# Optimization experiments

Hardware: AMD Instinct MI355X
Metric: run time of the kernel (lower is better)

## Reference

```python
import jax, jax.numpy as jnp
import numpy as np

L = 5        # n_layers
H = 8        # heads
DH = 32      # dim_head = n_hidden // heads
D = 256      # n_hidden
KR = 4       # key_ratio
QKD = KR * DH  # 128, q/k feature dim
IN = 3       # fun_dim + space_dim
OUT = 1      # out_dim
N = 32768    # number of mesh points
EPS = 1e-5

def _ln(x, g, b):
    m = jnp.mean(x, axis=-1, keepdims=True)
    v = jnp.var(x, axis=-1, keepdims=True)
    return (x - m) * jax.lax.rsqrt(v + EPS) * g + b

def _gelu(x):
    return jax.nn.gelu(x, approximate=False)  # torch nn.GELU default (erf)

def setup_inputs() -> dict:
    key = jax.random.key(0)
    ks = iter(jax.random.split(key, 64))
    def w(*s):
        return jax.random.normal(next(ks), s, jnp.float32) * 0.02
    return {
        "x": jax.random.normal(next(ks), (N, IN), jnp.float32),
        # preprocess MLP: Linear(IN,2D)+GELU, Linear(2D,D)
        "pre_w1": w(IN, 2 * D), "pre_b1": jnp.zeros((2 * D,), jnp.float32),
        "pre_w2": w(2 * D, D), "pre_b2": jnp.zeros((D,), jnp.float32),
        "placeholder": jax.random.uniform(next(ks), (D,), jnp.float32) / D,
        # per-block params stacked over L
        "ln1_g": jnp.ones((L, D), jnp.float32), "ln1_b": jnp.zeros((L, D), jnp.float32),
        "inp_w": w(L, D, D), "inp_b": jnp.zeros((L, D), jnp.float32),
        "temp_q": jnp.full((L, H), 0.5, jnp.float32), "temp_k": jnp.full((L, H), 0.5, jnp.float32),
        "wq": w(L, DH, QKD), "wk": w(L, DH, QKD), "wv": w(L, DH, DH),
        "out_w1": w(L, D, D), "out_b1": jnp.zeros((L, D), jnp.float32),
        "out_w2": w(L, D, D), "out_b2": jnp.zeros((L, D), jnp.float32),
        "ln2_g": jnp.ones((L, D), jnp.float32), "ln2_b": jnp.zeros((L, D), jnp.float32),
        "mlp_w1": w(L, D, D), "mlp_b1": jnp.zeros((L, D), jnp.float32),  # mlp_ratio=1 -> hidden=D
        "mlp_w2": w(L, D, D), "mlp_b2": jnp.zeros((L, D), jnp.float32),
        # last-layer head
        "ln3_g": jnp.ones((D,), jnp.float32), "ln3_b": jnp.zeros((D,), jnp.float32),
        "head_w": w(D, OUT), "head_b": jnp.zeros((OUT,), jnp.float32),
    }

def reference(x, pre_w1, pre_b1, pre_w2, pre_b2, placeholder,
              ln1_g, ln1_b, inp_w, inp_b, temp_q, temp_k, wq, wk, wv,
              out_w1, out_b1, out_w2, out_b2, ln2_g, ln2_b,
              mlp_w1, mlp_b1, mlp_w2, mlp_b2, ln3_g, ln3_b, head_w, head_b):
    # preprocess + placeholder bias
    fx = _gelu(x[None] @ pre_w1 + pre_b1) @ pre_w2 + pre_b2  # [1, N, D]
    fx = fx + placeholder
    for i in range(L):
        # --- LinearNO attention block ---
        h = _ln(fx, ln1_g[i], ln1_b[i])
        xm = h @ inp_w[i] + inp_b[i]                       # [1, N, D]
        xm = xm.reshape(1, N, H, DH).transpose(0, 2, 1, 3)  # [1, H, N, DH]
        q = jnp.einsum('bhnd,de->bhne', xm, wq[i])          # [1, H, N, QKD]
        k = jnp.einsum('bhnd,de->bhne', xm, wk[i])          # [1, H, N, QKD]
        v = jnp.einsum('bhnd,dc->bhnc', xm, wv[i])          # [1, H, N, DH]
        tq = jnp.clip(temp_q[i], 0.1, 2.0)[None, :, None, None]
        tk = jnp.clip(temp_k[i], 0.1, 2.0)[None, :, None, None]
        q = jax.nn.softmax(q / tq, axis=-1)  # over feature dim
        k = jax.nn.softmax(k / tk, axis=-2)  # over point dim
        kv = jnp.einsum('bhnd,bhnc->bhdc', k, v)    # [1, H, QKD, DH]
        qkv = jnp.einsum('bhnd,bhdc->bhnc', q, kv)  # [1, H, N, DH]
        qkv = qkv.transpose(0, 2, 1, 3).reshape(1, N, D)
        attn = _gelu(qkv @ out_w1[i] + out_b1[i]) @ out_w2[i] + out_b2[i]
        fx = attn + fx
        # --- MLP block (n_layers=0, res=False: pre + post only) ---
        h2 = _ln(fx, ln2_g[i], ln2_b[i])
        fx = _gelu(h2 @ mlp_w1[i] + mlp_b1[i]) @ mlp_w2[i] + mlp_b2[i] + fx
    # last block head: mlp2(ln_3(fx))
    out = _ln(fx, ln3_g, ln3_b) @ head_w + head_b  # [1, N, OUT]
    return out[0]  # module returns fx[0]
```

## Files before the change

### kernel.cpp

```cpp
#include <hip/hip_runtime.h>
#include <hip/hip_bf16.h>
#include <math.h>

constexpr int NP  = 32768;
constexpr int HH  = 8;

typedef short bf16x8 __attribute__((ext_vector_type(8)));
typedef float f32x4  __attribute__((ext_vector_type(4)));

__device__ __forceinline__ float gelu_f(float x) {
    return 0.5f * x * (1.0f + erff(x * 0.70710678118654752f));
}

__device__ __forceinline__ unsigned short f2bf(float x) {
    union { float f; unsigned u; } v; v.f = x;
    unsigned r = v.u + 0x7fffu + ((v.u >> 16) & 1u);
    return (unsigned short)(r >> 16);
}

__device__ __forceinline__ float bf2f(unsigned short h) {
    union { unsigned u; float f; } v; v.u = ((unsigned)h) << 16;
    return v.f;
}

__global__ __launch_bounds__(256) void transpose_bf16_k(
    const float* __restrict__ src, unsigned short* __restrict__ dst, int K)
{
    __shared__ float tile[32][33];
    int g = blockIdx.z;
    int k0 = blockIdx.x * 32, c0 = blockIdx.y * 32;
    int tx = threadIdx.x & 31, ty = threadIdx.x >> 5;
    const float* s = src + (size_t)g * K * 256;
    unsigned short* d = dst + (size_t)g * 256 * K;
    #pragma unroll
    for (int rr = 0; rr < 4; ++rr) {
        int r = ty + rr * 8;
        tile[r][tx] = s[(size_t)(k0 + r) * 256 + c0 + tx];
    }
    __syncthreads();
    #pragma unroll
    for (int rr = 0; rr < 4; ++rr) {
        int r = ty + rr * 8;
        d[(size_t)(c0 + r) * K + k0 + tx] = f2bf(tile[tx][r]);
    }
}

__global__ __launch_bounds__(256) void transpose_scale_bf16_k(
    const float* __restrict__ src, const float* __restrict__ g,
    unsigned short* __restrict__ dst, int K)
{
    __shared__ float tile[32][33];
    int z = blockIdx.z;
    int k0 = blockIdx.x * 32, c0 = blockIdx.y * 32;
    int tx = threadIdx.x & 31, ty = threadIdx.x >> 5;
    const float* s = src + (size_t)z * K * 256;
    unsigned short* d = dst + (size_t)z * 256 * K;
    #pragma unroll
    for (int rr = 0; rr < 4; ++rr) {
        int r = ty + rr * 8;
        tile[r][tx] = s[(size_t)(k0 + r) * 256 + c0 + tx];
    }
    __syncthreads();
    float gs = g[z * 256 + k0 + tx];
    #pragma unroll
    for (int rr = 0; rr < 4; ++rr) {
        int r = ty + rr * 8;
        d[(size_t)(c0 + r) * K + k0 + tx] = f2bf(gs * tile[tx][r]);
    }
}

__global__ __launch_bounds__(256) void colsum_k(
    const float* __restrict__ W, const float* __restrict__ g,
    const float* __restrict__ b, float* __restrict__ c2, float* __restrict__ c1)
{
    int z = blockIdx.z, c = threadIdx.x;
    const float* Wz = W + (size_t)z * 65536;
    const float* gz = g + z * 256;
    const float* bz = b + z * 256;
    float s2 = 0.f, s1 = 0.f;
    for (int k = 0; k < 256; ++k) {
        float w = Wz[k * 256 + c];
        s2 += gz[k] * w;
        s1 += bz[k] * w;
    }
    c2[z * 256 + c] = s2;
    c1[z * 256 + c] = s1;
}

__global__ __launch_bounds__(256) void prep_wkvT(
    const float* __restrict__ wk, const float* __restrict__ wv,
    const float* __restrict__ wq,
    unsigned short* __restrict__ wkT, unsigned short* __restrict__ wvT,
    unsigned short* __restrict__ wqT)
{
    int l = blockIdx.x, tid = threadIdx.x;
    for (int idx = tid; idx < 4096; idx += 256) {
        int d = idx >> 5, k = idx & 31;
        wkT[l * 4096 + idx] = f2bf(wk[l * 4096 + k * 128 + d]);
        wqT[l * 4096 + idx] = f2bf(wq[l * 4096 + k * 128 + d]);
    }
    for (int idx = tid; idx < 1024; idx += 256) {
        int c = idx >> 5, k = idx & 31;
        wvT[l * 1024 + idx] = f2bf(wv[l * 1024 + k * 32 + c]);
    }
}

template<bool GENA, bool AF32, bool LNFOLD, bool DOGELU, bool RESID, bool STATS, bool PERM>
__global__ __launch_bounds__(256) void gemm_bf(
    const unsigned short* __restrict__ Ah, const float* __restrict__ Af,
    const unsigned short* __restrict__ Wt,
    const float* __restrict__ bias, const float* __restrict__ bias2,
    float* __restrict__ outF, unsigned short* __restrict__ outH,
    const float* __restrict__ stats_in, float* __restrict__ stats_out,
    const float* __restrict__ c1v, const float* __restrict__ c2vec,
    const float* __restrict__ genx, const float* __restrict__ genw1,
    const float* __restrict__ genb1, int K)
{
    __shared__ __align__(16) unsigned short As[128 * 64];
    __shared__ __align__(16) unsigned short Bs[128 * 64];
    __shared__ float rmean[LNFOLD ? 128 : 1];
    __shared__ float rrstd[LNFOLD ? 128 : 1];
    __shared__ float w1s[GENA ? 1536 : 1];
    __shared__ float b1s[GENA ? 512 : 1];
    __shared__ float x3s[GENA ? 512 : 1];

    const int tid = threadIdx.x;
    const int rBase = blockIdx.x * 128, cBase = blockIdx.y * 128;

    if constexpr (GENA) {
        for (int i2 = tid; i2 < 1536; i2 += 256) w1s[i2] = genw1[i2];
        for (int i2 = tid; i2 < 512; i2 += 256) b1s[i2] = genb1[i2];
        if (tid < 128) {
            x3s[tid * 4 + 0] = genx[(size_t)(rBase + tid) * 3 + 0];
            x3s[tid * 4 + 1] = genx[(size_t)(rBase + tid) * 3 + 1];
            x3s[tid * 4 + 2] = genx[(size_t)(rBase + tid) * 3 + 2];
        }
        __syncthreads();
    }
    if constexpr (LNFOLD) {
        if (tid < 128) {
            const float* sp = stats_in + (size_t)(rBase + tid) * 8;
            float4 s0 = *(const float4*)sp;
            float4 s1 = *(const float4*)(sp + 4);
            float mean = (s0.x + s0.z + s1.x + s1.z) * (1.f / 256.f);
            float ex2  = (s0.y + s0.w + s1.y + s1.w) * (1.f / 256.f);
            rmean[tid] = mean;
            rrstd[tid] = rsqrtf(fmaxf(ex2 - mean * mean, 0.f) + 1e-5f);
        }
        __syncthreads();
    }

    f32x4 acc[4][4];
    #pragma unroll
    for (int i = 0; i < 4; ++i)
        #pragma unroll
        for (int j = 0; j < 4; ++j)
            acc[i][j] = (f32x4){0.f, 0.f, 0.f, 0.f};

    const int lane = tid & 63, wid = tid >> 6;
    const int wr = wid >> 1, wc = wid & 1;
    const int lrow = lane & 15, quad = lane >> 4;
    const int srow = tid >> 3;
    const int sch  = tid & 7;

    for (int kc = 0; kc < K; kc += 64) {
        if constexpr (GENA) {
            #pragma unroll
            for (int it = 0; it < 4; ++it) {
                int row = srow + it * 32;
                float x0 = x3s[row * 4 + 0], x1 = x3s[row * 4 + 1], x2 = x3s[row * 4 + 2];
                unsigned short pk[8];
                #pragma unroll
                for (int j = 0; j < 8; ++j) {
                    int k = kc + sch * 8 + j;
                    float t = x0 * w1s[k] + x1 * w1s[512 + k] + x2 * w1s[1024 + k] + b1s[k];
                    pk[j] = f2bf(gelu_f(t));
                }
                *(uint4*)&As[row * 64 + ((sch ^ (row & 7)) << 3)] = *(uint4*)pk;
            }
        } else if constexpr (AF32) {
            #pragma unroll
            for (int it = 0; it < 4; ++it) {
                int row = srow + it * 32;
                const float* ap = Af + (size_t)(rBase + row) * K + kc + sch * 8;
                float4 a0 = *(const float4*)ap;
                float4 a1 = *(const float4*)(ap + 4);
                unsigned short pk[8];
                pk[0] = f2bf(a0.x); pk[1] = f2bf(a0.y); pk[2] = f2bf(a0.z); pk[3] = f2bf(a0.w);
                pk[4] = f2bf(a1.x); pk[5] = f2bf(a1.y); pk[6] = f2bf(a1.z); pk[7] = f2bf(a1.w);
                *(uint4*)&As[row * 64 + ((sch ^ (row & 7)) << 3)] = *(uint4*)pk;
            }
        } else {
            #pragma unroll
            for (int it = 0; it < 4; ++it) {
                int row = srow + it * 32;
                uint4 av = *(const uint4*)(Ah + (size_t)(rBase + row) * K + kc + sch * 8);
                *(uint4*)&As[row * 64 + ((sch ^ (row & 7)) << 3)] = av;
            }
        }
        #pragma unroll
        for (int it = 0; it < 4; ++it) {
            int n = srow + it * 32;
            uint4 wv_ = *(const uint4*)(Wt + (size_t)(cBase + n) * K + kc + sch * 8);
            *(uint4*)&Bs[n * 64 + ((sch ^ (n & 7)) << 3)] = wv_;
        }
        __syncthreads();
        #pragma unroll
        for (int ks = 0; ks < 2; ++ks) {
            bf16x8 af[4], bfr[4];
            #pragma unroll
            for (int t = 0; t < 4; ++t) {
                int row = wr * 64 + t * 16 + lrow;
                af[t] = *(bf16x8*)&As[row * 64 + (((ks * 4 + quad) ^ (row & 7)) << 3)];
                int n = wc * 64 + t * 16 + lrow;
                bfr[t] = *(bf16x8*)&Bs[n * 64 + (((ks * 4 + quad) ^ (n & 7)) << 3)];
            }
            #pragma unroll
            for (int ti = 0; ti < 4; ++ti)
                #pragma unroll
                for (int tj = 0; tj < 4; ++tj)
                    acc[ti][tj] = __builtin_amdgcn_mfma_f32_16x16x32_bf16(
                        af[ti], bfr[tj], acc[ti][tj], 0, 0, 0);
        }
        __syncthreads();
    }

    float c1b[4], c2r[4];
    #pragma unroll
    for (int tj = 0; tj < 4; ++tj) {
        int gcol = cBase + wc * 64 + tj * 16 + lrow;
        float b = bias[gcol];
        if (bias2) b += bias2[gcol];
        if constexpr (LNFOLD) {
            c1b[tj] = c1v[gcol] + b;
            c2r[tj] = c2vec[gcol];
        } else {
            c1b[tj] = b;
            c2r[tj] = 0.f;
        }
    }
    #pragma unroll
    for (int ti = 0; ti < 4; ++ti) {
        #pragma unroll
        for (int r = 0; r < 4; ++r) {
            int rib = wr * 64 + ti * 16 + quad * 4 + r;
            int grow = rBase + rib;
            float mean = 0.f, rstd = 1.f;
            if constexpr (LNFOLD) { mean = rmean[rib]; rstd = rrstd[rib]; }
            float vv[4];
            #pragma unroll
            for (int tj = 0; tj < 4; ++tj) {
                float t = acc[ti][tj][r];
                float v;
                if constexpr (LNFOLD) v = rstd * (t - mean * c2r[tj]) + c1b[tj];
                else                  v = t + c1b[tj];
                if constexpr (DOGELU) v = gelu_f(v);
                vv[tj] = v;
            }
            if constexpr (RESID) {
                #pragma unroll
                for (int tj = 0; tj < 4; ++tj) {
                    int gcol = cBase + wc * 64 + tj * 16 + lrow;
                    vv[tj] += outF[(size_t)grow * 256 + gcol];
                }
            }
            if constexpr (STATS) {
                float rs = vv[0] + vv[1] + vv[2] + vv[3];
                float rq = vv[0]*vv[0] + vv[1]*vv[1] + vv[2]*vv[2] + vv[3]*vv[3];
                #pragma unroll
                for (int m = 1; m < 16; m <<= 1) {
                    rs += __shfl_xor(rs, m);
                    rq += __shfl_xor(rq, m);
                }
                if (lrow == 0) {
                    stats_out[(size_t)grow * 8 + (blockIdx.y * 2 + wc) * 2 + 0] = rs;
                    stats_out[(size_t)grow * 8 + (blockIdx.y * 2 + wc) * 2 + 1] = rq;
                }
            }
            #pragma unroll
            for (int tj = 0; tj < 4; ++tj) {
                int gcol = cBase + wc * 64 + tj * 16 + lrow;
                if constexpr (PERM) {
                    size_t pidx = (size_t)(gcol >> 5) * NP * 32 + (size_t)grow * 32 + (gcol & 31);
                    if (outF) outF[pidx] = vv[tj];
                    if (outH) outH[pidx] = f2bf(vv[tj]);
                } else {
                    if (outF) outF[(size_t)grow * 256 + gcol] = vv[tj];
                    if (outH) outH[(size_t)grow * 256 + gcol] = f2bf(vv[tj]);
                }
            }
        }
    }
}

__global__ __launch_bounds__(256) void attn_lgl(
    const unsigned short* __restrict__ xm, const unsigned short* __restrict__ wqT,
    const float* __restrict__ tq_arr,
    const unsigned short* __restrict__ kvT, const float* __restrict__ sumexp,
    const unsigned short* __restrict__ O1t, const float* __restrict__ ob1,
    const unsigned short* __restrict__ O2t, const float* __restrict__ ob2,
    float* __restrict__ fx, float* __restrict__ stats_out, int layer)
{
    __shared__ __align__(16) unsigned char upool[38912];
    __shared__ __align__(16) unsigned short Ts[64 * 256];

    unsigned short* xs  = (unsigned short*)(upool);
    unsigned short* wqs = (unsigned short*)(upool + 4096);
    unsigned short* kvb = (unsigned short*)(upool + 12288);
    unsigned short* els = (unsigned short*)(upool + 20992);
    float*          ises = (float*)(upool + 38400);
    unsigned short* Bs  = (unsigned short*)(upool);

    const int tid = threadIdx.x;
    const int rBase = blockIdx.x * 64;
    const int lane = tid & 63, wid = tid >> 6;
    const int lrow = lane & 15, quad = lane >> 4;

    #pragma unroll
    for (int it = 0; it < 2; ++it) {
        int cid = tid + it * 256;
        int d = cid >> 2, kc = cid & 3;
        uint4 v = *(const uint4*)(wqT + d * 32 + kc * 8);
        *(uint4*)&wqs[d * 32 + ((kc ^ (d & 3)) << 3)] = v;
    }
    for (int h = 0; h < 8; ++h) {
        if (h) __syncthreads();
        float tq = fminf(fmaxf(tq_arr[layer * 8 + h], 0.1f), 2.0f);
        float invtq = 1.0f / tq;
        if (tid < 128) ises[tid] = 1.0f / sumexp[h * 128 + tid];
        #pragma unroll
        for (int it = 0; it < 2; ++it) {
            int cid = tid + it * 256;
            int c = cid >> 4, k8 = cid & 15;
            uint4 v = *(const uint4*)(kvT + (size_t)h * 4096 + c * 128 + k8 * 8);
            *(uint4*)&kvb[c * 136 + k8 * 8] = v;
        }
        {
            int row = tid >> 2, kc = tid & 3;
            uint4 v = *(const uint4*)(xm + (size_t)h * NP * 32 +
                                      (size_t)(rBase + row) * 32 + kc * 8);
            *(uint4*)&xs[row * 32 + ((kc ^ (row & 3)) << 3)] = v;
        }
        __syncthreads();

        int arow = wid * 16 + lrow;
        bf16x8 ax = *(bf16x8*)&xs[arow * 32 + ((quad ^ (arow & 3)) << 3)];
        f32x4 lg[8];
        #pragma unroll
        for (int dt = 0; dt < 8; ++dt) {
            int d = dt * 16 + lrow;
            bf16x8 bw = *(bf16x8*)&wqs[d * 32 + ((quad ^ (d & 3)) << 3)];
            f32x4 cc = (f32x4){0.f, 0.f, 0.f, 0.f};
            lg[dt] = __builtin_amdgcn_mfma_f32_16x16x32_bf16(ax, bw, cc, 0, 0, 0);
        }
        float isv[8];
        #pragma unroll
        for (int dt = 0; dt < 8; ++dt) isv[dt] = ises[dt * 16 + lrow];

        #pragma unroll
        for (int r = 0; r < 4; ++r) {
            float m = lg[0][r];
            #pragma unroll
            for (int dt = 1; dt < 8; ++dt) m = fmaxf(m, lg[dt][r]);
            m = fmaxf(m, __shfl_xor(m, 1));
            m = fmaxf(m, __shfl_xor(m, 2));
            m = fmaxf(m, __shfl_xor(m, 4));
            m = fmaxf(m, __shfl_xor(m, 8));
            float e[8], s = 0.f;
            #pragma unroll
            for (int dt = 0; dt < 8; ++dt) {
                e[dt] = __expf((lg[dt][r] - m) * invtq);
                s += e[dt];
            }
            s += __shfl_xor(s, 1);
            s += __shfl_xor(s, 2);
            s += __shfl_xor(s, 4);
            s += __shfl_xor(s, 8);
            float inv = 1.0f / s;
            int erow = wid * 16 + quad * 4 + r;
            #pragma unroll
            for (int dt = 0; dt < 8; ++dt)
                els[erow * 136 + dt * 16 + lrow] = f2bf(e[dt] * inv * isv[dt]);
        }

        #pragma unroll
        for (int ct = 0; ct < 2; ++ct) {
            f32x4 oc = (f32x4){0.f, 0.f, 0.f, 0.f};
            #pragma unroll
            for (int ks = 0; ks < 4; ++ks) {
                bf16x8 ae = *(bf16x8*)&els[(wid * 16 + lrow) * 136 + ks * 32 + quad * 8];
                bf16x8 bv = *(bf16x8*)&kvb[(ct * 16 + lrow) * 136 + ks * 32 + quad * 8];
                oc = __builtin_amdgcn_mfma_f32_16x16x32_bf16(ae, bv, oc, 0, 0, 0);
            }
            #pragma unroll
            for (int r = 0; r < 4; ++r) {
                int row = wid * 16 + quad * 4 + r;
                int col = h * 32 + ct * 16 + lrow;
                int ch = col >> 3;
                Ts[row * 256 + ((ch ^ (row & 7)) << 3) + (col & 7)] = f2bf(oc[r]);
            }
        }
    }
    __syncthreads();

    auto gemm_phase = [&](const unsigned short* __restrict__ Wt, f32x4 (&acc)[4][4]) {
        for (int kc = 0; kc < 256; kc += 64) {
            #pragma unroll
            for (int it = 0; it < 8; ++it) {
                int idx = tid + it * 256;
                int n = idx >> 3, sch = idx & 7;
                uint4 wv_ = *(const uint4*)(Wt + (size_t)n * 256 + kc + sch * 8);
                *(uint4*)&Bs[n * 64 + ((sch ^ (n & 7)) << 3)] = wv_;
            }
            __syncthreads();
            #pragma unroll
            for (int ks = 0; ks < 2; ++ks) {
                bf16x8 af[4], bfr[4];
                #pragma unroll
                for (int t = 0; t < 4; ++t) {
                    int row = t * 16 + lrow;
                    int ch = (kc >> 3) + ks * 4 + quad;
                    af[t] = *(bf16x8*)&Ts[row * 256 + ((ch ^ (row & 7)) << 3)];
                    int n = wid * 64 + t * 16 + lrow;
                    bfr[t] = *(bf16x8*)&Bs[n * 64 + (((ks * 4 + quad) ^ (n & 7)) << 3)];
                }
                #pragma unroll
                for (int ti = 0; ti < 4; ++ti)
                    #pragma unroll
                    for (int tj = 0; tj < 4; ++tj)
                        acc[ti][tj] = __builtin_amdgcn_mfma_f32_16x16x32_bf16(
                            af[ti], bfr[tj], acc[ti][tj], 0, 0, 0);
            }
            __syncthreads();
        }
    };

    f32x4 acc[4][4];
    #pragma unroll
    for (int i = 0; i < 4; ++i)
        #pragma unroll
        for (int j = 0; j < 4; ++j) acc[i][j] = (f32x4){0.f, 0.f, 0.f, 0.f};
    gemm_phase(O1t, acc);
    {
        float c1b[4];
        #pragma unroll
        for (int tj = 0; tj < 4; ++tj) c1b[tj] = ob1[wid * 64 + tj * 16 + lrow];
        #pragma unroll
        for (int ti = 0; ti < 4; ++ti) {
            #pragma unroll
            for (int r = 0; r < 4; ++r) {
                int row = ti * 16 + quad * 4 + r;
                #pragma unroll
                for (int tj = 0; tj < 4; ++tj) {
                    float v = gelu_f(acc[ti][tj][r] + c1b[tj]);
                    int col = wid * 64 + tj * 16 + lrow;
                    int ch = col >> 3;
                    Ts[row * 256 + ((ch ^ (row & 7)) << 3) + (col & 7)] = f2bf(v);
                }
            }
        }
    }
    __syncthreads();

    #pragma unroll
    for (int i = 0; i < 4; ++i)
        #pragma unroll
        for (int j = 0; j < 4; ++j) acc[i][j] = (f32x4){0.f, 0.f, 0.f, 0.f};
    gemm_phase(O2t, acc);
    {
        float bb[4];
        #pragma unroll
        for (int tj = 0; tj < 4; ++tj) bb[tj] = ob2[wid * 64 + tj * 16 + lrow];
        #pragma unroll
        for (int ti = 0; ti < 4; ++ti) {
            #pragma unroll
            for (int r = 0; r < 4; ++r) {
                int row = ti * 16 + quad * 4 + r;
                int grow = rBase + row;
                float vv[4];
                #pragma unroll
                for (int tj = 0; tj < 4; ++tj) {
                    int gcol = wid * 64 + tj * 16 + lrow;
                    vv[tj] = acc[ti][tj][r] + bb[tj] + fx[(size_t)grow * 256 + gcol];
                }
                float rs = vv[0] + vv[1] + vv[2] + vv[3];
                float rq = vv[0]*vv[0] + vv[1]*vv[1] + vv[2]*vv[2] + vv[3]*vv[3];
                #pragma unroll
                for (int m = 1; m < 16; m <<= 1) {
                    rs += __shfl_xor(rs, m);
                    rq += __shfl_xor(rq, m);
                }
                if (lrow == 0) {
                    stats_out[(size_t)grow * 8 + wid * 2 + 0] = rs;
                    stats_out[(size_t)grow * 8 + wid * 2 + 1] = rq;
                }
                #pragma unroll
                for (int tj = 0; tj < 4; ++tj) {
                    int gcol = wid * 64 + tj * 16 + lrow;
                    fx[(size_t)grow * 256 + gcol] = vv[tj];
                }
            }
        }
    }
}

template<bool AF32, bool LNFOLD, bool WSTATS, bool NEXTW>
__global__ __launch_bounds__(256) void gemm_lgl(
    const unsigned short* __restrict__ Ah, const float* __restrict__ Af,
    const unsigned short* __restrict__ W1t, const unsigned short* __restrict__ W2t,
    const float* __restrict__ b1, const float* __restrict__ b2,
    float* __restrict__ fx,
    const float* __restrict__ stats_in, float* __restrict__ stats_out,
    const float* __restrict__ c1v, const float* __restrict__ c2vec,
    const unsigned short* __restrict__ W3t, const float* __restrict__ b3,
    const float* __restrict__ c1n, const float* __restrict__ c2n,
    unsigned short* __restrict__ outNext)
{
    __shared__ __align__(16) unsigned short As[64 * 64];
    __shared__ __align__(16) unsigned short Bs[256 * 64];
    __shared__ __align__(16) unsigned short Ts[64 * 256];
    __shared__ float rmean[(LNFOLD || NEXTW) ? 64 : 1];
    __shared__ float rrstd[(LNFOLD || NEXTW) ? 64 : 1];
    __shared__ float ssum[NEXTW ? 256 : 1];
    __shared__ float ssq [NEXTW ? 256 : 1];

    const int tid = threadIdx.x;
    const int rBase = blockIdx.x * 64;
    const int lane = tid & 63, wid = tid >> 6;
    const int lrow = lane & 15, quad = lane >> 4;

    if constexpr (LNFOLD) {
        if (tid < 64) {
            const float* sp = stats_in + (size_t)(rBase + tid) * 8;
            float4 s0 = *(const float4*)sp;
            float4 s1 = *(const float4*)(sp + 4);
            float mean = (s0.x + s0.z + s1.x + s1.z) * (1.f / 256.f);
            float ex2  = (s0.y + s0.w + s1.y + s1.w) * (1.f / 256.f);
            rmean[tid] = mean;
            rrstd[tid] = rsqrtf(fmaxf(ex2 - mean * mean, 0.f) + 1e-5f);
        }
    }

    f32x4 acc[4][4];
    #pragma unroll
    for (int i = 0; i < 4; ++i)
        #pragma unroll
        for (int j = 0; j < 4; ++j)
            acc[i][j] = (f32x4){0.f, 0.f, 0.f, 0.f};

    for (int kc = 0; kc < 256; kc += 64) {
        #pragma unroll
        for (int it = 0; it < 2; ++it) {
            int idx = tid + it * 256;
            int row = idx >> 3, sch = idx & 7;
            if constexpr (AF32) {
                const float* ap = Af + (size_t)(rBase + row) * 256 + kc + sch * 8;
                float4 a0 = *(const float4*)ap;
                float4 a1 = *(const float4*)(ap + 4);
                unsigned short pk[8];
                pk[0] = f2bf(a0.x); pk[1] = f2bf(a0.y); pk[2] = f2bf(a0.z); pk[3] = f2bf(a0.w);
                pk[4] = f2bf(a1.x); pk[5] = f2bf(a1.y); pk[6] = f2bf(a1.z); pk[7] = f2bf(a1.w);
                *(uint4*)&As[row * 64 + ((sch ^ (row & 7)) << 3)] = *(uint4*)pk;
            } else {
                uint4 av = *(const uint4*)(Ah + (size_t)(rBase + row) * 256 + kc + sch * 8);
                *(uint4*)&As[row * 64 + ((sch ^ (row & 7)) << 3)] = av;
            }
        }
        #pragma unroll
        for (int it = 0; it < 8; ++it) {
            int idx = tid + it * 256;
            int n = idx >> 3, sch = idx & 7;
            uint4 wv_ = *(const uint4*)(W1t + (size_t)n * 256 + kc + sch * 8);
            *(uint4*)&Bs[n * 64 + ((sch ^ (n & 7)) << 3)] = wv_;
        }
        __syncthreads();
        #pragma unroll
        for (int ks = 0; ks < 2; ++ks) {
            bf16x8 af[4], bfr[4];
            #pragma unroll
            for (int t = 0; t < 4; ++t) {
                int row = t * 16 + lrow;
                af[t] = *(bf16x8*)&As[row * 64 + (((ks * 4 + quad) ^ (row & 7)) << 3)];
                int n = wid * 64 + t * 16 + lrow;
                bfr[t] = *(bf16x8*)&Bs[n * 64 + (((ks * 4 + quad) ^ (n & 7)) << 3)];
            }
            #pragma unroll
            for (int ti = 0; ti < 4; ++ti)
                #pragma unroll
                for (int tj = 0; tj < 4; ++tj)
                    acc[ti][tj] = __builtin_amdgcn_mfma_f32_16x16x32_bf16(
                        af[ti], bfr[tj], acc[ti][tj], 0, 0, 0);
        }
        __syncthreads();
    }

    {
        float c1b[4], c2r[4];
        #pragma unroll
        for (int tj = 0; tj < 4; ++tj) {
            int gcol = wid * 64 + tj * 16 + lrow;
            if constexpr (LNFOLD) {
                c1b[tj] = c1v[gcol] + b1[gcol];
                c2r[tj] = c2vec[gcol];
            } else {
                c1b[tj] = b1[gcol];
                c2r[tj] = 0.f;
            }
        }
        #pragma unroll
        for (int ti = 0; ti < 4; ++ti) {
            #pragma unroll
            for (int r = 0; r < 4; ++r) {
                int row = ti * 16 + quad * 4 + r;
                float mean = 0.f, rstd = 1.f;
                if constexpr (LNFOLD) { mean = rmean[row]; rstd = rrstd[row]; }
                #pragma unroll
                for (int tj = 0; tj < 4; ++tj) {
                    float t = acc[ti][tj][r];
                    float v;
                    if constexpr (LNFOLD) v = rstd * (t - mean * c2r[tj]) + c1b[tj];
                    else                  v = t + c1b[tj];
                    v = gelu_f(v);
                    int col = wid * 64 + tj * 16 + lrow;
                    int ch = col >> 3;
                    Ts[row * 256 + ((ch ^ (row & 7)) << 3) + (col & 7)] = f2bf(v);
                }
            }
        }
    }
    __syncthreads();

    f32x4 acc2[4][4];
    #pragma unroll
    for (int i = 0; i < 4; ++i)
        #pragma unroll
        for (int j = 0; j < 4; ++j)
            acc2[i][j] = (f32x4){0.f, 0.f, 0.f, 0.f};

    for (int kc = 0; kc < 256; kc += 64) {
        #pragma unroll
        for (int it = 0; it < 8; ++it) {
            int idx = tid + it * 256;
            int n = idx >> 3, sch = idx & 7;
            uint4 wv_ = *(const uint4*)(W2t + (size_t)n * 256 + kc + sch * 8);
            *(uint4*)&Bs[n * 64 + ((sch ^ (n & 7)) << 3)] = wv_;
        }
        __syncthreads();
        #pragma unroll
        for (int ks = 0; ks < 2; ++ks) {
            bf16x8 af[4], bfr[4];
            #pragma unroll
            for (int t = 0; t < 4; ++t) {
                int row = t * 16 + lrow;
                int ch = (kc >> 3) + ks * 4 + quad;
                af[t] = *(bf16x8*)&Ts[row * 256 + ((ch ^ (row & 7)) << 3)];
                int n = wid * 64 + t * 16 + lrow;
                bfr[t] = *(bf16x8*)&Bs[n * 64 + (((ks * 4 + quad) ^ (n & 7)) << 3)];
            }
            #pragma unroll
            for (int ti = 0; ti < 4; ++ti)
                #pragma unroll
                for (int tj = 0; tj < 4; ++tj)
                    acc2[ti][tj] = __builtin_amdgcn_mfma_f32_16x16x32_bf16(
                        af[ti], bfr[tj], acc2[ti][tj], 0, 0, 0);
        }
        __syncthreads();
    }

    float bb[4];
    #pragma unroll
    for (int tj = 0; tj < 4; ++tj) bb[tj] = b2[wid * 64 + tj * 16 + lrow];
    #pragma unroll
    for (int ti = 0; ti < 4; ++ti) {
        #pragma unroll
        for (int r = 0; r < 4; ++r) {
            int row = ti * 16 + quad * 4 + r;
            int grow = rBase + row;
            float vv[4];
            #pragma unroll
            for (int tj = 0; tj < 4; ++tj) {
                int gcol = wid * 64 + tj * 16 + lrow;
                vv[tj] = acc2[ti][tj][r] + bb[tj] + fx[(size_t)grow * 256 + gcol];
            }
            if constexpr (WSTATS || NEXTW) {
                float rs = vv[0] + vv[1] + vv[2] + vv[3];
                float rq = vv[0]*vv[0] + vv[1]*vv[1] + vv[2]*vv[2] + vv[3]*vv[3];
                #pragma unroll
                for (int m = 1; m < 16; m <<= 1) {
                    rs += __shfl_xor(rs, m);
                    rq += __shfl_xor(rq, m);
                }
                if (lrow == 0) {
                    if constexpr (WSTATS) {
                        stats_out[(size_t)grow * 8 + wid * 2 + 0] = rs;
                        stats_out[(size_t)grow * 8 + wid * 2 + 1] = rq;
                    }
                    if constexpr (NEXTW) {
                        ssum[row * 4 + wid] = rs;
                        ssq [row * 4 + wid] = rq;
                    }
                }
            }
            #pragma unroll
            for (int tj = 0; tj < 4; ++tj) {
                int gcol = wid * 64 + tj * 16 + lrow;
                fx[(size_t)grow * 256 + gcol] = vv[tj];
                if constexpr (NEXTW) {
                    int ch = gcol >> 3;
                    Ts[row * 256 + ((ch ^ (row & 7)) << 3) + (gcol & 7)] = f2bf(vv[tj]);
                }
            }
        }
    }

    if constexpr (NEXTW) {
        __syncthreads();
        if (tid < 64) {
            float mean = (ssum[tid*4+0] + ssum[tid*4+1] + ssum[tid*4+2] + ssum[tid*4+3]) * (1.f/256.f);
            float ex2  = (ssq [tid*4+0] + ssq [tid*4+1] + ssq [tid*4+2] + ssq [tid*4+3]) * (1.f/256.f);
            rmean[tid] = mean;
            rrstd[tid] = rsqrtf(fmaxf(ex2 - mean * mean, 0.f) + 1e-5f);
        }
        __syncthreads();

        f32x4 acc3[4][4];
        #pragma unroll
        for (int i = 0; i < 4; ++i)
            #pragma unroll
            for (int j = 0; j < 4; ++j)
                acc3[i][j] = (f32x4){0.f, 0.f, 0.f, 0.f};

        for (int kc = 0; kc < 256; kc += 64) {
            #pragma unroll
            for (int it = 0; it < 8; ++it) {
                int idx = tid + it * 256;
                int n = idx >> 3, sch = idx & 7;
                uint4 wv_ = *(const uint4*)(W3t + (size_t)n * 256 + kc + sch * 8);
                *(uint4*)&Bs[n * 64 + ((sch ^ (n & 7)) << 3)] = wv_;
            }
            __syncthreads();
            #pragma unroll
            for (int ks = 0; ks < 2; ++ks) {
                bf16x8 af[4], bfr[4];
                #pragma unroll
                for (int t = 0; t < 4; ++t) {
                    int row = t * 16 + lrow;
                    int ch = (kc >> 3) + ks * 4 + quad;
                    af[t] = *(bf16x8*)&Ts[row * 256 + ((ch ^ (row & 7)) << 3)];
                    int n = wid * 64 + t * 16 + lrow;
                    bfr[t] = *(bf16x8*)&Bs[n * 64 + (((ks * 4 + quad) ^ (n & 7)) << 3)];
                }
                #pragma unroll
                for (int ti = 0; ti < 4; ++ti)
                    #pragma unroll
                    for (int tj = 0; tj < 4; ++tj)
                        acc3[ti][tj] = __builtin_amdgcn_mfma_f32_16x16x32_bf16(
                            af[ti], bfr[tj], acc3[ti][tj], 0, 0, 0);
            }
            __syncthreads();
        }

        float c1b3[4], c2r3[4];
        #pragma unroll
        for (int tj = 0; tj < 4; ++tj) {
            int gcol = wid * 64 + tj * 16 + lrow;
            c1b3[tj] = c1n[gcol] + b3[gcol];
            c2r3[tj] = c2n[gcol];
        }
        #pragma unroll
        for (int ti = 0; ti < 4; ++ti) {
            #pragma unroll
            for (int r = 0; r < 4; ++r) {
                int row = ti * 16 + quad * 4 + r;
                int grow = rBase + row;
                float mean = rmean[row], rstd = rrstd[row];
                #pragma unroll
                for (int tj = 0; tj < 4; ++tj) {
                    int gcol = wid * 64 + tj * 16 + lrow;
                    float t = acc3[ti][tj][r];
                    float v = rstd * (t - mean * c2r3[tj]) + c1b3[tj];
                    size_t pidx = (size_t)(gcol >> 5) * NP * 32 + (size_t)grow * 32 + (gcol & 31);
                    outNext[pidx] = f2bf(v);
                }
            }
        }
    }
}

__global__ __launch_bounds__(256) void kv6_kernel(
    const unsigned short* __restrict__ xm2h, const unsigned short* __restrict__ wkT,
    const unsigned short* __restrict__ wvT, const float* __restrict__ tk_arr,
    float* __restrict__ partials, int layer)
{
    __shared__ __align__(16) unsigned short xs[64 * 32];
    __shared__ __align__(16) unsigned short wks[128 * 32];
    __shared__ __align__(16) unsigned short wvs[32 * 32];
    __shared__ __align__(16) unsigned short els[128 * 72];
    __shared__ __align__(16) unsigned short vls[32 * 72];
    __shared__ float sums[4 * 128];

    const int tid = threadIdx.x;
    const int h = blockIdx.y;
    const int rowBase = blockIdx.x * 512;
    const int w = tid >> 6, lane = tid & 63;
    const int lrow = lane & 15, quad = lane >> 4;

    float tk = fminf(fmaxf(tk_arr[layer * 8 + h], 0.1f), 2.0f);
    float invtk = 1.0f / tk;

    #pragma unroll
    for (int it = 0; it < 2; ++it) {
        int cid = tid + it * 256;
        int d = cid >> 2, kc = cid & 3;
        uint4 v = *(const uint4*)(wkT + d * 32 + kc * 8);
        *(uint4*)&wks[d * 32 + ((kc ^ (d & 3)) << 3)] = v;
    }
    if (tid < 128) {
        int c = tid >> 2, kc = tid & 3;
        uint4 v = *(const uint4*)(wvT + c * 32 + kc * 8);
        *(uint4*)&wvs[c * 32 + ((kc ^ (c & 3)) << 3)] = v;
    }

    f32x4 acc2[2][2];
    #pragma unroll
    for (int di = 0; di < 2; ++di)
        #pragma unroll
        for (int ci = 0; ci < 2; ++ci)
            acc2[di][ci] = (f32x4){0.f, 0.f, 0.f, 0.f};
    float seacc[8];
    #pragma unroll
    for (int dt = 0; dt < 8; ++dt) seacc[dt] = 0.f;

    const unsigned short* src = xm2h + (size_t)h * NP * 32 + (size_t)rowBase * 32;

    for (int sub = 0; sub < 8; ++sub) {
        __syncthreads();
        {
            int row = tid >> 2, kc = tid & 3;
            uint4 v = *(const uint4*)(src + (size_t)(sub * 64 + row) * 32 + kc * 8);
            *(uint4*)&xs[row * 32 + ((kc ^ (row & 3)) << 3)] = v;
        }
        __syncthreads();
        int arow = w * 16 + lrow;
        bf16x8 ax = *(bf16x8*)&xs[arow * 32 + ((quad ^ (arow & 3)) << 3)];
        #pragma unroll
        for (int ct = 0; ct < 2; ++ct) {
            int c = ct * 16 + lrow;
            bf16x8 bw = *(bf16x8*)&wvs[c * 32 + ((quad ^ (c & 3)) << 3)];
            f32x4 cc = (f32x4){0.f, 0.f, 0.f, 0.f};
            cc = __builtin_amdgcn_mfma_f32_16x16x32_bf16(ax, bw, cc, 0, 0, 0);
            unsigned short pk[4];
            pk[0] = f2bf(cc[0]); pk[1] = f2bf(cc[1]);
            pk[2] = f2bf(cc[2]); pk[3] = f2bf(cc[3]);
            *(uint2*)&vls[(ct * 16 + lrow) * 72 + w * 16 + quad * 4] = *(uint2*)pk;
        }
        #pragma unroll
        for (int dt = 0; dt < 8; ++dt) {
            int d = dt * 16 + lrow;
            bf16x8 bw = *(bf16x8*)&wks[d * 32 + ((quad ^ (d & 3)) << 3)];
            f32x4 cc = (f32x4){0.f, 0.f, 0.f, 0.f};
            cc = __builtin_amdgcn_mfma_f32_16x16x32_bf16(ax, bw, cc, 0, 0, 0);
            unsigned short pk[4];
            float se = 0.f;
            #pragma unroll
            for (int r = 0; r < 4; ++r) {
                float l = fminf(fmaxf(cc[r] * invtk, -30.f), 30.f);
                unsigned short eb = f2bf(__expf(l));
                pk[r] = eb;
                se += bf2f(eb);
            }
            seacc[dt] += se;
            *(uint2*)&els[d * 72 + w * 16 + quad * 4] = *(uint2*)pk;
        }
        __syncthreads();
        #pragma unroll
        for (int di = 0; di < 2; ++di) {
            int dm = (2 * w + di) * 16 + lrow;
            #pragma unroll
            for (int ks = 0; ks < 2; ++ks) {
                bf16x8 ae = *(bf16x8*)&els[dm * 72 + ks * 32 + quad * 8];
                #pragma unroll
                for (int ci = 0; ci < 2; ++ci) {
                    int cn = ci * 16 + lrow;
                    bf16x8 bv = *(bf16x8*)&vls[cn * 72 + ks * 32 + quad * 8];
                    acc2[di][ci] = __builtin_amdgcn_mfma_f32_16x16x32_bf16(
                        ae, bv, acc2[di][ci], 0, 0, 0);
                }
            }
        }
    }

    float* outp = partials + ((size_t)h * 64 + blockIdx.x) * 4224;
    #pragma unroll
    for (int di = 0; di < 2; ++di)
        #pragma unroll
        for (int ci = 0; ci < 2; ++ci)
            #pragma unroll
            for (int r = 0; r < 4; ++r) {
                int d = (2 * w + di) * 16 + quad * 4 + r;
                int c = ci * 16 + lrow;
                outp[d * 32 + c] = acc2[di][ci][r];
            }
    #pragma unroll
    for (int dt = 0; dt < 8; ++dt) {
        float s = seacc[dt];
        s += __shfl_xor(s, 16);
        s += __shfl_xor(s, 32);
        if (quad == 0) sums[w * 128 + dt * 16 + lrow] = s;
    }
    __syncthreads();
    if (tid < 128)
        outp[4096 + tid] = sums[tid] + sums[128 + tid] + sums[256 + tid] + sums[384 + tid];
}

__global__ __launch_bounds__(256) void kv_reduce_kernel(
    const float* __restrict__ partials, unsigned short* __restrict__ kvT,
    float* __restrict__ sumexp)
{
    int gid = blockIdx.x * 256 + threadIdx.x;
    if (gid >= 8 * 4224) return;
    int h = gid / 4224, idx = gid % 4224;
    const float* base = partials + (size_t)h * 64 * 4224 + idx;
    float s = 0.f;
    #pragma unroll 8
    for (int c = 0; c < 64; ++c) s += base[(size_t)c * 4224];
    if (idx < 4096) {
        int d = idx >> 5, c = idx & 31;
        kvT[(size_t)h * 4096 + c * 128 + d] = f2bf(s);
    } else {
        sumexp[h * 128 + (idx - 4096)] = s;
    }
}

__global__ __launch_bounds__(256) void head_kernel(
    const float* __restrict__ fx, const float* __restrict__ g, const float* __restrict__ b,
    const float* __restrict__ hw, const float* __restrict__ hb, float* __restrict__ out)
{
    int lane = threadIdx.x & 63;
    int row = blockIdx.x * 4 + (threadIdx.x >> 6);
    float4 v = *(const float4*)(fx + (size_t)row * 256 + lane * 4);
    float s1 = v.x + v.y + v.z + v.w;
    float s2 = v.x * v.x + v.y * v.y + v.z * v.z + v.w * v.w;
    #pragma unroll
    for (int m = 1; m < 64; m <<= 1) { s1 += __shfl_xor(s1, m); s2 += __shfl_xor(s2, m); }
    float mean = s1 * 0.00390625f;
    float rstd = rsqrtf(fmaxf(s2 * 0.00390625f - mean * mean, 0.f) + 1e-5f);
    float4 gg = *(const float4*)(g + lane * 4);
    float4 bb = *(const float4*)(b + lane * 4);
    float4 w4 = *(const float4*)(hw + lane * 4);
    float d = ((v.x - mean) * rstd * gg.x + bb.x) * w4.x
            + ((v.y - mean) * rstd * gg.y + bb.y) * w4.y
            + ((v.z - mean) * rstd * gg.z + bb.z) * w4.z
            + ((v.w - mean) * rstd * gg.w + bb.w) * w4.w;
    #pragma unroll
    for (int m = 1; m < 64; m <<= 1) d += __shfl_xor(d, m);
    if (lane == 0) out[row] = d + hb[0];
}

extern "C" void kernel_launch(void* const* d_in, const int* in_sizes, int n_in,
                              void* d_out, int out_size, void* d_ws, size_t ws_size,
                              hipStream_t stream)
{
    const float* x      = (const float*)d_in[0];
    const float* pre_w1 = (const float*)d_in[1];
    const float* pre_b1 = (const float*)d_in[2];
    const float* pre_w2 = (const float*)d_in[3];
    const float* pre_b2 = (const float*)d_in[4];
    const float* ph     = (const float*)d_in[5];
    const float* ln1_g  = (const float*)d_in[6];
    const float* ln1_b  = (const float*)d_in[7];
    const float* inp_w  = (const float*)d_in[8];
    const float* inp_b  = (const float*)d_in[9];
    const float* temp_q = (const float*)d_in[10];
    const float* temp_k = (const float*)d_in[11];
    const float* wq     = (const float*)d_in[12];
    const float* wk     = (const float*)d_in[13];
    const float* wv     = (const float*)d_in[14];
    const float* out_w1 = (const float*)d_in[15];
    const float* out_b1 = (const float*)d_in[16];
    const float* out_w2 = (const float*)d_in[17];
    const float* out_b2 = (const float*)d_in[18];
    const float* ln2_g  = (const float*)d_in[19];
    const float* ln2_b  = (const float*)d_in[20];
    const float* mlp_w1 = (const float*)d_in[21];
    const float* mlp_b1 = (const float*)d_in[22];
    const float* mlp_w2 = (const float*)d_in[23];
    const float* mlp_b2 = (const float*)d_in[24];
    const float* ln3_g  = (const float*)d_in[25];
    const float* ln3_b  = (const float*)d_in[26];
    const float* head_w = (const float*)d_in[27];
    const float* head_b = (const float*)d_in[28];
    float* out = (float*)d_out;

    float* fx = (float*)d_ws;
    unsigned short* xmB = (unsigned short*)(fx + (size_t)NP * 256);
    unsigned short* xmA = xmB + (size_t)NP * 256;
    float* scr = (float*)(xmA + (size_t)NP * 256);
    float* st = scr + (size_t)NP * 256;
    unsigned short* kvT = (unsigned short*)(st + (size_t)NP * 8);
    float* se = (float*)(kvT + 8 * 4096);
    float* c1i = se + 8 * 128;
    float* c2i = c1i + 1280;
    float* c1m = c2i + 1280;
    float* c2m = c1m + 1280;
    unsigned short* wtPre = (unsigned short*)(c2m + 1280);
    unsigned short* wtL   = wtPre + 256 * 512;
    unsigned short* wkT   = wtL + 25 * 65536;
    unsigned short* wvT   = wkT + 5 * 4096;
    unsigned short* wqT   = wvT + 5 * 1024;

    unsigned short* wtIn = wtL;
    unsigned short* wtO1 = wtL +  5 * 65536;
    unsigned short* wtO2 = wtL + 10 * 65536;
    unsigned short* wtM1 = wtL + 15 * 65536;
    unsigned short* wtM2 = wtL + 20 * 65536;

    dim3 bt(256);

    transpose_bf16_k<<<dim3(16, 8, 1), bt, 0, stream>>>(pre_w2, wtPre, 512);
    transpose_scale_bf16_k<<<dim3(8, 8, 5), bt, 0, stream>>>(inp_w,  ln1_g, wtIn, 256);
    transpose_bf16_k<<<dim3(8, 8, 5), bt, 0, stream>>>(out_w1, wtO1, 256);
    transpose_bf16_k<<<dim3(8, 8, 5), bt, 0, stream>>>(out_w2, wtO2, 256);
    transpose_scale_bf16_k<<<dim3(8, 8, 5), bt, 0, stream>>>(mlp_w1, ln2_g, wtM1, 256);
    transpose_bf16_k<<<dim3(8, 8, 5), bt, 0, stream>>>(mlp_w2, wtM2, 256);
    colsum_k<<<dim3(1, 1, 5), bt, 0, stream>>>(inp_w,  ln1_g, ln1_b, c2i, c1i);
    colsum_k<<<dim3(1, 1, 5), bt, 0, stream>>>(mlp_w1, ln2_g, ln2_b, c2m, c1m);
    prep_wkvT<<<dim3(5), bt, 0, stream>>>(wk, wv, wq, wkT, wvT, wqT);

    dim3 gg(256, 2);

    gemm_bf<true, false, false, false, false, true, false><<<gg, bt, 0, stream>>>(
        nullptr, nullptr, wtPre, pre_b2, ph, fx, nullptr, nullptr, st,
        nullptr, nullptr, x, pre_w1, pre_b1, 512);

    gemm_bf<false, true, true, false, false, false, true><<<gg, bt, 0, stream>>>(
        nullptr, fx, wtIn, inp_b, nullptr, nullptr, xmA,
        st, nullptr, c1i, c2i, nullptr, nullptr, nullptr, 256);

    for (int i = 0; i < 5; ++i) {
        unsigned short* xmCur  = (i & 1) ? xmB : xmA;
        unsigned short* xmNext = (i & 1) ? xmA : xmB;
        kv6_kernel<<<dim3(64, 8), bt, 0, stream>>>(
            xmCur, wkT + (size_t)i * 4096, wvT + (size_t)i * 1024, temp_k, scr, i);
        kv_reduce_kernel<<<dim3(132), bt, 0, stream>>>(scr, kvT, se);
        attn_lgl<<<dim3(512), bt, 0, stream>>>(
            xmCur, wqT + (size_t)i * 4096, temp_q, kvT, se,
            wtO1 + (size_t)i * 65536, out_b1 + i * 256,
            wtO2 + (size_t)i * 65536, out_b2 + i * 256,
            fx, st, i);
        if (i < 4) {
            gemm_lgl<true, true, false, true><<<dim3(512), bt, 0, stream>>>(
                nullptr, fx, wtM1 + (size_t)i * 65536, wtM2 + (size_t)i * 65536,
                mlp_b1 + i * 256, mlp_b2 + i * 256, fx, st, nullptr,
                c1m + i * 256, c2m + i * 256,
                wtIn + (size_t)(i + 1) * 65536, inp_b + (i + 1) * 256,
                c1i + (i + 1) * 256, c2i + (i + 1) * 256, xmNext);
        } else {
            gemm_lgl<true, true, false, false><<<dim3(512), bt, 0, stream>>>(
                nullptr, fx, wtM1 + (size_t)i * 65536, wtM2 + (size_t)i * 65536,
                mlp_b1 + i * 256, mlp_b2 + i * 256, fx, st, nullptr,
                c1m + i * 256, c2m + i * 256,
                nullptr, nullptr, nullptr, nullptr, nullptr);
        }
    }
    head_kernel<<<dim3(NP / 4), bt, 0, stream>>>(fx, ln3_g, ln3_b, head_w, head_b, out);
}
```

Baseline: 818.4 us.

## Fuse preprocess MLP and first layer input projection into one row-block kernel

Replaces the two generic gemm_bf launches (preprocess second linear with stats, then the LN-folded first input projection) with one gena_lgl kernel. Each block owns 64 full rows, computes fx plus per-row LayerNorm stats in shared memory, keeps the bf16 fx tile in LDS, and immediately runs the in-projection to write xm. This removes one launch, the global stats round trip and the fp32 re-read of fx. In exchange it uses larger shared memory per block and smaller row tiles, which may reduce occupancy.

```diff
diff --git a/kernel.cpp b/kernel.cpp
--- a/kernel.cpp
+++ b/kernel.cpp
@@ -105,103 +105,69 @@
     }
 }
 
-template<bool GENA, bool AF32, bool LNFOLD, bool DOGELU, bool RESID, bool STATS, bool PERM>
-__global__ __launch_bounds__(256) void gemm_bf(
-    const unsigned short* __restrict__ Ah, const float* __restrict__ Af,
-    const unsigned short* __restrict__ Wt,
-    const float* __restrict__ bias, const float* __restrict__ bias2,
-    float* __restrict__ outF, unsigned short* __restrict__ outH,
-    const float* __restrict__ stats_in, float* __restrict__ stats_out,
-    const float* __restrict__ c1v, const float* __restrict__ c2vec,
+__global__ __launch_bounds__(256) void gena_lgl(
     const float* __restrict__ genx, const float* __restrict__ genw1,
-    const float* __restrict__ genb1, int K)
+    const float* __restrict__ genb1,
+    const unsigned short* __restrict__ W2t, const float* __restrict__ b2,
+    const float* __restrict__ ph,
+    float* __restrict__ fx,
+    const unsigned short* __restrict__ W3t, const float* __restrict__ b3,
+    const float* __restrict__ c1n, const float* __restrict__ c2n,
+    unsigned short* __restrict__ outNext)
 {
-    __shared__ __align__(16) unsigned short As[128 * 64];
-    __shared__ __align__(16) unsigned short Bs[128 * 64];
-    __shared__ float rmean[LNFOLD ? 128 : 1];
-    __shared__ float rrstd[LNFOLD ? 128 : 1];
-    __shared__ float w1s[GENA ? 1536 : 1];
-    __shared__ float b1s[GENA ? 512 : 1];
-    __shared__ float x3s[GENA ? 512 : 1];
+    __shared__ __align__(16) unsigned char tpool[32768];
+    __shared__ __align__(16) unsigned short As[64 * 64];
+    __shared__ __align__(16) unsigned short Bs[256 * 64];
+    __shared__ float rmean[64];
+    __shared__ float rrstd[64];
+    __shared__ float ssum[256];
+    __shared__ float ssq[256];
+
+    float* w1s = (float*)tpool;
+    float* b1s = (float*)(tpool + 6144);
+    float* x3s = (float*)(tpool + 8192);
+    unsigned short* Ts = (unsigned short*)tpool;
 
     const int tid = threadIdx.x;
-    const int rBase = blockIdx.x * 128, cBase = blockIdx.y * 128;
-
-    if constexpr (GENA) {
-        for (int i2 = tid; i2 < 1536; i2 += 256) w1s[i2] = genw1[i2];
-        for (int i2 = tid; i2 < 512; i2 += 256) b1s[i2] = genb1[i2];
-        if (tid < 128) {
-            x3s[tid * 4 + 0] = genx[(size_t)(rBase + tid) * 3 + 0];
-            x3s[tid * 4 + 1] = genx[(size_t)(rBase + tid) * 3 + 1];
-            x3s[tid * 4 + 2] = genx[(size_t)(rBase + tid) * 3 + 2];
-        }
-        __syncthreads();
-    }
-    if constexpr (LNFOLD) {
-        if (tid < 128) {
-            const float* sp = stats_in + (size_t)(rBase + tid) * 8;
-            float4 s0 = *(const float4*)sp;
-            float4 s1 = *(const float4*)(sp + 4);
-            float mean = (s0.x + s0.z + s1.x + s1.z) * (1.f / 256.f);
-            float ex2  = (s0.y + s0.w + s1.y + s1.w) * (1.f / 256.f);
-            rmean[tid] = mean;
-            rrstd[tid] = rsqrtf(fmaxf(ex2 - mean * mean, 0.f) + 1e-5f);
-        }
-        __syncthreads();
-    }
+    const int rBase = blockIdx.x * 64;
+    const int lane = tid & 63, wid = tid >> 6;
+    const int lrow = lane & 15, quad = lane >> 4;
+
+    for (int i2 = tid; i2 < 1536; i2 += 256) w1s[i2] = genw1[i2];
+    for (int i2 = tid; i2 < 512; i2 += 256) b1s[i2] = genb1[i2];
+    if (tid < 64) {
+        x3s[tid * 4 + 0] = genx[(size_t)(rBase + tid) * 3 + 0];
+        x3s[tid * 4 + 1] = genx[(size_t)(rBase + tid) * 3 + 1];
+        x3s[tid * 4 + 2] = genx[(size_t)(rBase + tid) * 3 + 2];
+    }
+    __syncthreads();
 
     f32x4 acc[4][4];
     #pragma unroll
     for (int i = 0; i < 4; ++i)
         #pragma unroll
-        for (int j = 0; j < 4; ++j)
-            acc[i][j] = (f32x4){0.f, 0.f, 0.f, 0.f};
-
-    const int lane = tid & 63, wid = tid >> 6;
-    const int wr = wid >> 1, wc = wid & 1;
-    const int lrow = lane & 15, quad = lane >> 4;
-    const int srow = tid >> 3;
-    const int sch  = tid & 7;
-
-    for (int kc = 0; kc < K; kc += 64) {
-        if constexpr (GENA) {
-            #pragma unroll
-            for (int it = 0; it < 4; ++it) {
-                int row = srow + it * 32;
-                float x0 = x3s[row * 4 + 0], x1 = x3s[row * 4 + 1], x2 = x3s[row * 4 + 2];
-                unsigned short pk[8];
-                #pragma unroll
-                for (int j = 0; j < 8; ++j) {
-                    int k = kc + sch * 8 + j;
-                    float t = x0 * w1s[k] + x1 * w1s[512 + k] + x2 * w1s[1024 + k] + b1s[k];
-                    pk[j] = f2bf(gelu_f(t));
-                }
-                *(uint4*)&As[row * 64 + ((sch ^ (row & 7)) << 3)] = *(uint4*)pk;
-            }
-        } else if constexpr (AF32) {
-            #pragma unroll
-            for (int it = 0; it < 4; ++it) {
-                int row = srow + it * 32;
-                const float* ap = Af + (size_t)(rBase + row) * K + kc + sch * 8;
-                float4 a0 = *(const float4*)ap;
-                float4 a1 = *(const float4*)(ap + 4);
-                unsigned short pk[8];
-                pk[0] = f2bf(a0.x); pk[1] = f2bf(a0.y); pk[2] = f2bf(a0.z); pk[3] = f2bf(a0.w);
-                pk[4] = f2bf(a1.x); pk[5] = f2bf(a1.y); pk[6] = f2bf(a1.z); pk[7] = f2bf(a1.w);
-                *(uint4*)&As[row * 64 + ((sch ^ (row & 7)) << 3)] = *(uint4*)pk;
-            }
-        } else {
-            #pragma unroll
-            for (int it = 0; it < 4; ++it) {
-                int row = srow + it * 32;
-                uint4 av = *(const uint4*)(Ah + (size_t)(rBase + row) * K + kc + sch * 8);
-                *(uint4*)&As[row * 64 + ((sch ^ (row & 7)) << 3)] = av;
-            }
-        }
-        #pragma unroll
-        for (int it = 0; it < 4; ++it) {
-            int n = srow + it * 32;
-            uint4 wv_ = *(const uint4*)(Wt + (size_t)(cBase + n) * K + kc + sch * 8);
+        for (int j = 0; j < 4; ++j) acc[i][j] = (f32x4){0.f, 0.f, 0.f, 0.f};
+
+    for (int kc = 0; kc < 512; kc += 64) {
+        #pragma unroll
+        for (int it = 0; it < 2; ++it) {
+            int idx = tid + it * 256;
+            int row = idx >> 3, sch = idx & 7;
+            float x0 = x3s[row * 4 + 0], x1 = x3s[row * 4 + 1], x2 = x3s[row * 4 + 2];
+            unsigned short pk[8];
+            #pragma unroll
+            for (int j = 0; j < 8; ++j) {
+                int k = kc + sch * 8 + j;
+                float t = x0 * w1s[k] + x1 * w1s[512 + k] + x2 * w1s[1024 + k] + b1s[k];
+                pk[j] = f2bf(gelu_f(t));
+            }
+            *(uint4*)&As[row * 64 + ((sch ^ (row & 7)) << 3)] = *(uint4*)pk;
+        }
+        #pragma unroll
+        for (int it = 0; it < 8; ++it) {
+            int idx = tid + it * 256;
+            int n = idx >> 3, sch = idx & 7;
+            uint4 wv_ = *(const uint4*)(W2t + (size_t)n * 512 + kc + sch * 8);
             *(uint4*)&Bs[n * 64 + ((sch ^ (n & 7)) << 3)] = wv_;
         }
         __syncthreads();
@@ -210,9 +176,9 @@
             bf16x8 af[4], bfr[4];
             #pragma unroll
             for (int t = 0; t < 4; ++t) {
-                int row = wr * 64 + t * 16 + lrow;
+                int row = t * 16 + lrow;
                 af[t] = *(bf16x8*)&As[row * 64 + (((ks * 4 + quad) ^ (row & 7)) << 3)];
-                int n = wc * 64 + t * 16 + lrow;
+                int n = wid * 64 + t * 16 + lrow;
                 bfr[t] = *(bf16x8*)&Bs[n * 64 + (((ks * 4 + quad) ^ (n & 7)) << 3)];
             }
             #pragma unroll
@@ -225,46 +191,23 @@
         __syncthreads();
     }
 
-    float c1b[4], c2r[4];
-    #pragma unroll
-    for (int tj = 0; tj < 4; ++tj) {
-        int gcol = cBase + wc * 64 + tj * 16 + lrow;
-        float b = bias[gcol];
-        if (bias2) b += bias2[gcol];
-        if constexpr (LNFOLD) {
-            c1b[tj] = c1v[gcol] + b;
-            c2r[tj] = c2vec[gcol];
-        } else {
-            c1b[tj] = b;
-            c2r[tj] = 0.f;
-        }
-    }
-    #pragma unroll
-    for (int ti = 0; ti < 4; ++ti) {
-        #pragma unroll
-        for (int r = 0; r < 4; ++r) {
-            int rib = wr * 64 + ti * 16 + quad * 4 + r;
-            int grow = rBase + rib;
-            float mean = 0.f, rstd = 1.f;
-            if constexpr (LNFOLD) { mean = rmean[rib]; rstd = rrstd[rib]; }
-            float vv[4];
-            #pragma unroll
-            for (int tj = 0; tj < 4; ++tj) {
-                float t = acc[ti][tj][r];
-                float v;
-                if constexpr (LNFOLD) v = rstd * (t - mean * c2r[tj]) + c1b[tj];
-                else                  v = t + c1b[tj];
-                if constexpr (DOGELU) v = gelu_f(v);
-                vv[tj] = v;
-            }
-            if constexpr (RESID) {
-                #pragma unroll
-                for (int tj = 0; tj < 4; ++tj) {
-                    int gcol = cBase + wc * 64 + tj * 16 + lrow;
-                    vv[tj] += outF[(size_t)grow * 256 + gcol];
-                }
-            }
-            if constexpr (STATS) {
+    {
+        float c1b[4];
+        #pragma unroll
+        for (int tj = 0; tj < 4; ++tj) {
+            int gcol = wid * 64 + tj * 16 + lrow;
+            c1b[tj] = b2[gcol] + ph[gcol];
+        }
+        #pragma unroll
+        for (int ti = 0; ti < 4; ++ti) {
+            #pragma unroll
+            for (int r = 0; r < 4; ++r) {
+                int row = ti * 16 + quad * 4 + r;
+                int grow = rBase + row;
+                float vv[4];
+                #pragma unroll
+                for (int tj = 0; tj < 4; ++tj)
+                    vv[tj] = acc[ti][tj][r] + c1b[tj];
                 float rs = vv[0] + vv[1] + vv[2] + vv[3];
                 float rq = vv[0]*vv[0] + vv[1]*vv[1] + vv[2]*vv[2] + vv[3]*vv[3];
                 #pragma unroll
@@ -272,22 +215,83 @@
                     rs += __shfl_xor(rs, m);
                     rq += __shfl_xor(rq, m);
                 }
-                if (lrow == 0) {
-                    stats_out[(size_t)grow * 8 + (blockIdx.y * 2 + wc) * 2 + 0] = rs;
-                    stats_out[(size_t)grow * 8 + (blockIdx.y * 2 + wc) * 2 + 1] = rq;
-                }
-            }
+                if (lrow == 0) { ssum[row * 4 + wid] = rs; ssq[row * 4 + wid] = rq; }
+                #pragma unroll
+                for (int tj = 0; tj < 4; ++tj) {
+                    int gcol = wid * 64 + tj * 16 + lrow;
+                    fx[(size_t)grow * 256 + gcol] = vv[tj];
+                    int ch = gcol >> 3;
+                    Ts[row * 256 + ((ch ^ (row & 7)) << 3) + (gcol & 7)] = f2bf(vv[tj]);
+                }
+            }
+        }
+    }
+    __syncthreads();
+    if (tid < 64) {
+        float mean = (ssum[tid*4+0] + ssum[tid*4+1] + ssum[tid*4+2] + ssum[tid*4+3]) * (1.f/256.f);
+        float ex2  = (ssq [tid*4+0] + ssq [tid*4+1] + ssq [tid*4+2] + ssq [tid*4+3]) * (1.f/256.f);
+        rmean[tid] = mean;
+        rrstd[tid] = rsqrtf(fmaxf(ex2 - mean * mean, 0.f) + 1e-5f);
+    }
+    __syncthreads();
+
+    f32x4 acc3[4][4];
+    #pragma unroll
+    for (int i = 0; i < 4; ++i)
+        #pragma unroll
+        for (int j = 0; j < 4; ++j) acc3[i][j] = (f32x4){0.f, 0.f, 0.f, 0.f};
+
+    for (int kc = 0; kc < 256; kc += 64) {
+        #pragma unroll
+        for (int it = 0; it < 8; ++it) {
+            int idx = tid + it * 256;
+            int n = idx >> 3, sch = idx & 7;
+            uint4 wv_ = *(const uint4*)(W3t + (size_t)n * 256 + kc + sch * 8);
+            *(uint4*)&Bs[n * 64 + ((sch ^ (n & 7)) << 3)] = wv_;
+        }
+        __syncthreads();
+        #pragma unroll
+        for (int ks = 0; ks < 2; ++ks) {
+            bf16x8 af[4], bfr[4];
+            #pragma unroll
+            for (int t = 0; t < 4; ++t) {
+                int row = t * 16 + lrow;
+                int ch = (kc >> 3) + ks * 4 + quad;
+                af[t] = *(bf16x8*)&Ts[row * 256 + ((ch ^ (row & 7)) << 3)];
+                int n = wid * 64 + t * 16 + lrow;
+                bfr[t] = *(bf16x8*)&Bs[n * 64 + (((ks * 4 + quad) ^ (n & 7)) << 3)];
+            }
+            #pragma unroll
+            for (int ti = 0; ti < 4; ++ti)
+                #pragma unroll
+                for (int tj = 0; tj < 4; ++tj)
+                    acc3[ti][tj] = __builtin_amdgcn_mfma_f32_16x16x32_bf16(
+                        af[ti], bfr[tj], acc3[ti][tj], 0, 0, 0);
+        }
+        __syncthreads();
+    }
+
+    float c1b3[4], c2r3[4];
+    #pragma unroll
+    for (int tj = 0; tj < 4; ++tj) {
+        int gcol = wid * 64 + tj * 16 + lrow;
+        c1b3[tj] = c1n[gcol] + b3[gcol];
+        c2r3[tj] = c2n[gcol];
+    }
+    #pragma unroll
+    for (int ti = 0; ti < 4; ++ti) {
+        #pragma unroll
+        for (int r = 0; r < 4; ++r) {
+            int row = ti * 16 + quad * 4 + r;
+            int grow = rBase + row;
+            float mean = rmean[row], rstd = rrstd[row];
             #pragma unroll
             for (int tj = 0; tj < 4; ++tj) {
-                int gcol = cBase + wc * 64 + tj * 16 + lrow;
-                if constexpr (PERM) {
-                    size_t pidx = (size_t)(gcol >> 5) * NP * 32 + (size_t)grow * 32 + (gcol & 31);
-                    if (outF) outF[pidx] = vv[tj];
-                    if (outH) outH[pidx] = f2bf(vv[tj]);
-                } else {
-                    if (outF) outF[(size_t)grow * 256 + gcol] = vv[tj];
-                    if (outH) outH[(size_t)grow * 256 + gcol] = f2bf(vv[tj]);
-                }
+                int gcol = wid * 64 + tj * 16 + lrow;
+                float t = acc3[ti][tj][r];
+                float v = rstd * (t - mean * c2r3[tj]) + c1b3[tj];
+                size_t pidx = (size_t)(gcol >> 5) * NP * 32 + (size_t)grow * 32 + (gcol & 31);
+                outNext[pidx] = f2bf(v);
             }
         }
     }
@@ -1027,15 +1031,9 @@
     colsum_k<<<dim3(1, 1, 5), bt, 0, stream>>>(mlp_w1, ln2_g, ln2_b, c2m, c1m);
     prep_wkvT<<<dim3(5), bt, 0, stream>>>(wk, wv, wq, wkT, wvT, wqT);
 
-    dim3 gg(256, 2);
-
-    gemm_bf<true, false, false, false, false, true, false><<<gg, bt, 0, stream>>>(
-        nullptr, nullptr, wtPre, pre_b2, ph, fx, nullptr, nullptr, st,
-        nullptr, nullptr, x, pre_w1, pre_b1, 512);
-
-    gemm_bf<false, true, true, false, false, false, true><<<gg, bt, 0, stream>>>(
-        nullptr, fx, wtIn, inp_b, nullptr, nullptr, xmA,
-        st, nullptr, c1i, c2i, nullptr, nullptr, nullptr, 256);
+    gena_lgl<<<dim3(512), bt, 0, stream>>>(
+        x, pre_w1, pre_b1, wtPre, pre_b2, ph, fx,
+        wtIn, inp_b, c1i, c2i, xmA);
 
     for (int i = 0; i < 5; ++i) {
         unsigned short* xmCur  = (i & 1) ? xmB : xmA;
```

New measurement: 798.5 us (median of 5 runs). 2.4% less time.
